# Kernel tuning notes

Measured on AMD Instinct MI355X. Metric: run time of the kernel, lower is better.

Reference implementation:

```python
import math
import jax, jax.numpy as jnp
import numpy as np

HEADS = 16
REL_WINDOW = 128


def setup_inputs() -> dict:
    key = jax.random.key(0)
    k1, k2, k3, k4, k5 = jax.random.split(key, 5)
    b, s, d = 2, 2048, 1024
    hd = d // HEADS          # 64
    R = 2 * REL_WINDOW + 1   # 257
    return {
        "x": jax.random.normal(k1, (b, s, d), dtype=jnp.float32),
        "Wqkv": jax.random.normal(k2, (3 * d, d), dtype=jnp.float32) * (1.0 / math.sqrt(d)),
        "bqkv": jax.random.normal(k3, (3 * d,), dtype=jnp.float32) * 0.02,
        "Wr": jax.random.normal(k4, (R, hd), dtype=jnp.float32) * (1.0 / math.sqrt(hd)),
        "br": jax.random.normal(k5, (R,), dtype=jnp.float32) * 0.02,
    }


def reference(x, Wqkv, bqkv, Wr, br):
    b, s, d = x.shape
    h = HEADS
    hd = d // h
    w = REL_WINDOW
    scale = math.sqrt(d / h)

    # qkv projection; torch view(b,s,h,3*hd) then chunk(3, dim=-1)
    qkv = (x @ Wqkv.T + bqkv).reshape(b, s, h, 3 * hd)
    q, k, v = jnp.split(qkv, 3, axis=-1)          # each [b,s,h,hd]
    q = q.transpose(0, 2, 1, 3)                   # [b,h,s,hd]
    k = k.transpose(0, 2, 1, 3)
    v = v.transpose(0, 2, 1, 3)

    # content scores
    content = jnp.einsum('bhik,bhjk->bhij', q, k) / scale  # [b,h,s,s]

    # relative position scores: project queries to R logits, gather per (i,j) offset
    idx = jnp.arange(s)
    offsets = jnp.clip(idx[None, :] - idx[:, None], -w, w) + w  # [s,s] in [0, 2w]
    rp = jnp.einsum('bhik,rk->bhir', q, Wr) + br               # [b,h,s,R]
    pos = jnp.take_along_axis(rp, jnp.broadcast_to(offsets, (b, h, s, s)), axis=-1)

    attn = jax.nn.softmax(content + pos, axis=-1)
    out = jnp.einsum('bhij,bhjk->bhik', attn, v)  # [b,h,s,hd]
    return out.transpose(0, 2, 1, 3).reshape(b, s, d)
```

## Files before the change

kernel.cpp:

```cpp
#include <hip/hip_runtime.h>

typedef short bfrag __attribute__((ext_vector_type(8)));
typedef float f32x4 __attribute__((ext_vector_type(4)));

#define MFMA16(a, b, c) __builtin_amdgcn_mfma_f32_16x16x32_bf16((a), (b), (c), 0, 0, 0)

#define SEQ   2048
#define DMOD  1024
#define NHEAD 16
#define HDIM  64
#define RSZ   257
#define RSTRIDE 260
#define RPADN 272
#define XN    (4096*1024)
#define WN    (3072*1024)
#define LOG2E 1.44269504f

__device__ __forceinline__ unsigned short f2bf(float f) {
  unsigned int u = __float_as_uint(f);
  u += 0x7FFFu + ((u >> 16) & 1u);
  return (unsigned short)(u >> 16);
}
__device__ __forceinline__ float bf2f(unsigned short u) {
  return __uint_as_float(((unsigned int)u) << 16);
}
__device__ __forceinline__ unsigned int pkbf(float a, float b) {
#if defined(__gfx950__)
  unsigned int r;
  asm("v_cvt_pk_bf16_f32 %0, %1, %2" : "=v"(r) : "v"(a), "v"(b));
  return r;
#else
  return (unsigned int)f2bf(a) | ((unsigned int)f2bf(b) << 16);
#endif
}
__device__ __forceinline__ float fexp2(float x) {
#if __has_builtin(__builtin_amdgcn_exp2f)
  return __builtin_amdgcn_exp2f(x);
#else
  return __expf(x * 0.69314718f);
#endif
}
__device__ __forceinline__ void gl2lds16(const void* g, void* l) {
  __builtin_amdgcn_global_load_lds(
      (__attribute__((address_space(1))) void*)(g),
      (__attribute__((address_space(3))) void*)(l), 16, 0, 0);
}

__global__ __launch_bounds__(256) void cast_all(const float* __restrict__ x,
                                                const float* __restrict__ Wqkv,
                                                const float* __restrict__ Wr,
                                                unsigned short* __restrict__ xb,
                                                unsigned short* __restrict__ wb,
                                                unsigned short* __restrict__ wrb) {
  int i = (blockIdx.x * 256 + threadIdx.x) * 4;
  if (i < XN) {
    float4 v = *(const float4*)(x + i);
    ushort4 o; o.x = f2bf(v.x); o.y = f2bf(v.y); o.z = f2bf(v.z); o.w = f2bf(v.w);
    *(ushort4*)(xb + i) = o;
  } else if (i < XN + WN) {
    int j = i - XN;
    float4 v = *(const float4*)(Wqkv + j);
    ushort4 o; o.x = f2bf(v.x); o.y = f2bf(v.y); o.z = f2bf(v.z); o.w = f2bf(v.w);
    *(ushort4*)(wb + j) = o;
  } else {
    int j = i - XN - WN;
    ushort4 o;
    unsigned short t[4];
#pragma unroll
    for (int k = 0; k < 4; ++k)
      t[k] = (j + k < RSZ * HDIM) ? f2bf(Wr[j + k]) : (unsigned short)0;
    o.x = t[0]; o.y = t[1]; o.z = t[2]; o.w = t[3];
    *(ushort4*)(wrb + j) = o;
  }
}

__global__ __launch_bounds__(256) void qkv_gemm(const unsigned short* __restrict__ xb,
                                                const unsigned short* __restrict__ wb,
                                                const float* __restrict__ bqkv,
                                                unsigned short* __restrict__ qb,
                                                unsigned short* __restrict__ kbuf,
                                                unsigned short* __restrict__ vtb) {
  __shared__ unsigned short SMEM[2 * 128 * 64];
  unsigned short* As = SMEM;
  unsigned short* Bs = SMEM + 128 * 64;
  unsigned short* Vtmp = SMEM;
  const int tid = threadIdx.x;
  const int m0 = blockIdx.y * 128, n0 = blockIdx.x * 128;
  const int wave = tid >> 6, lane = tid & 63;
  const int q4 = lane >> 4, l16 = lane & 15;
  const int wm = (wave & 1) * 64, wn = (wave >> 1) * 64;
  const int sw = l16 & 7;

  f32x4 acc[4][4];
#pragma unroll
  for (int rt = 0; rt < 4; ++rt)
#pragma unroll
    for (int ct = 0; ct < 4; ++ct) acc[rt][ct] = (f32x4){0.f, 0.f, 0.f, 0.f};

  for (int k0 = 0; k0 < DMOD; k0 += 64) {
#pragma unroll
    for (int it = 0; it < 4; ++it) {
      int ch = it * 256 + tid;
      int r = ch >> 3, cl = (ch & 7) ^ (r & 7);
      gl2lds16(xb + (size_t)(m0 + r) * DMOD + k0 + cl * 8, As + ch * 8);
      gl2lds16(wb + (size_t)(n0 + r) * DMOD + k0 + cl * 8, Bs + ch * 8);
    }
    __syncthreads();
#pragma unroll
    for (int ks = 0; ks < 2; ++ks) {
      bfrag af[4], bf[4];
#pragma unroll
      for (int rt = 0; rt < 4; ++rt)
        af[rt] = *(const bfrag*)(As + (wm + rt * 16 + l16) * 64 + ((ks * 4 + q4) ^ sw) * 8);
#pragma unroll
      for (int ct = 0; ct < 4; ++ct)
        bf[ct] = *(const bfrag*)(Bs + (wn + ct * 16 + l16) * 64 + ((ks * 4 + q4) ^ sw) * 8);
#pragma unroll
      for (int rt = 0; rt < 4; ++rt)
#pragma unroll
        for (int ct = 0; ct < 4; ++ct)
          acc[rt][ct] = MFMA16(bf[ct], af[rt], acc[rt][ct]);
    }
    __syncthreads();
  }

  const int batch = m0 >> 11;
  const int sbase = m0 & 2047;
  const int r3 = blockIdx.x % 3;
  const bool hasV = (r3 != 0);
  const int nv0 = n0 + ((r3 == 2) ? 64 : 0);

#pragma unroll
  for (int ct = 0; ct < 4; ++ct) {
    int ng = n0 + wn + ct * 16 + q4 * 4;
    int hh = ng / 192;
    int rem = ng - hh * 192;
    int t = rem >> 6, dd = rem & 63;
    float4 b4 = *(const float4*)(bqkv + ng);
    if (t < 2) {
      unsigned short* dst = (t == 0) ? qb : kbuf;
      size_t rowo = ((size_t)(batch * NHEAD + hh)) * SEQ + sbase;
#pragma unroll
      for (int rt = 0; rt < 4; ++rt) {
        int m = wm + rt * 16 + l16;
        uint2 pv;
        pv.x = pkbf(acc[rt][ct][0] + b4.x, acc[rt][ct][1] + b4.y);
        pv.y = pkbf(acc[rt][ct][2] + b4.z, acc[rt][ct][3] + b4.w);
        *(uint2*)(dst + (rowo + m) * HDIM + dd) = pv;
      }
    } else {
#pragma unroll
      for (int rt = 0; rt < 4; ++rt) {
        int m = wm + rt * 16 + l16;
        Vtmp[(dd + 0) * 136 + m] = f2bf(acc[rt][ct][0] + b4.x);
        Vtmp[(dd + 1) * 136 + m] = f2bf(acc[rt][ct][1] + b4.y);
        Vtmp[(dd + 2) * 136 + m] = f2bf(acc[rt][ct][2] + b4.z);
        Vtmp[(dd + 3) * 136 + m] = f2bf(acc[rt][ct][3] + b4.w);
      }
    }
  }

  if (hasV) {
    __syncthreads();
    const int hh = nv0 / 192;
    unsigned short* vdst = vtb + ((size_t)(batch * NHEAD + hh)) * HDIM * SEQ;
#pragma unroll
    for (int it = 0; it < 4; ++it) {
      int u = it * 256 + tid;
      int dd = u >> 4, mc = u & 15;
      bfrag val = *(const bfrag*)(Vtmp + dd * 136 + mc * 8);
      *(bfrag*)(vdst + (size_t)dd * SEQ + sbase + mc * 8) = val;
    }
  }
}

__global__ __launch_bounds__(256) void rp_gemm(const unsigned short* __restrict__ qb,
                                               const unsigned short* __restrict__ wrb,
                                               const float* __restrict__ br,
                                               unsigned short* __restrict__ rp16) {
  __shared__ unsigned short WrS[RPADN * HDIM];
  __shared__ unsigned short Qs[64 * HDIM];
  const int tid = threadIdx.x;
  const size_t row0 = (size_t)blockIdx.x * 64;

  for (int i = tid; i < RPADN * HDIM / 8; i += 256)
    *(uint4*)(&WrS[i * 8]) = *(const uint4*)(&wrb[i * 8]);
  for (int i = tid; i < 512; i += 256)
    *(uint4*)(&Qs[i * 8]) = *(const uint4*)(&qb[row0 * HDIM + i * 8]);
  __syncthreads();

  const int wave = tid >> 6, lane = tid & 63;
  const int q4 = lane >> 4, l16 = lane & 15;

  bfrag af0 = *(const bfrag*)(Qs + (wave * 16 + l16) * 64 + q4 * 8);
  bfrag af1 = *(const bfrag*)(Qs + (wave * 16 + l16) * 64 + 32 + q4 * 8);

  unsigned short* rrow = rp16 + (row0 + wave * 16 + l16) * RSTRIDE;
  const float br256 = br[256];

#pragma unroll 4
  for (int ct = 0; ct < 16; ++ct) {
    f32x4 acc = (f32x4){0.f, 0.f, 0.f, 0.f};
    bfrag w0 = *(const bfrag*)(WrS + (ct * 16 + l16) * 64 + q4 * 8);
    bfrag w1 = *(const bfrag*)(WrS + (ct * 16 + l16) * 64 + 32 + q4 * 8);
    acc = MFMA16(w0, af0, acc);
    acc = MFMA16(w1, af1, acc);
    int r = ct * 16 + q4 * 4;
    float4 b4 = *(const float4*)(br + r);
    uint2 pv;
    pv.x = pkbf((acc[0] + b4.x) * LOG2E, (acc[1] + b4.y) * LOG2E);
    pv.y = pkbf((acc[2] + b4.z) * LOG2E, (acc[3] + b4.w) * LOG2E);
    *(uint2*)(rrow + r) = pv;
  }
  {
    f32x4 acc = (f32x4){0.f, 0.f, 0.f, 0.f};
    bfrag w0 = *(const bfrag*)(WrS + (256 + l16) * 64 + q4 * 8);
    bfrag w1 = *(const bfrag*)(WrS + (256 + l16) * 64 + 32 + q4 * 8);
    acc = MFMA16(w0, af0, acc);
    acc = MFMA16(w1, af1, acc);
    if (q4 == 0)
      rrow[256] = f2bf((acc[0] + br256) * LOG2E);
  }
}

__global__ __launch_bounds__(256) void flash_attn(const unsigned short* __restrict__ qb,
                                                  const unsigned short* __restrict__ kbuf,
                                                  const unsigned short* __restrict__ vtb,
                                                  const unsigned short* __restrict__ rp16,
                                                  float* __restrict__ out) {
  __shared__ unsigned short Ks[2][64 * 64];
  __shared__ unsigned short Vs[2][64 * 64];
  __shared__ unsigned short Ps[64 * 64];

  const int tid = threadIdx.x;
  const int orig = blockIdx.x;
  const int slot = orig >> 3;
  const int bh = (orig & 7) * 4 + (slot >> 5);
  const int i0 = (slot & 31) << 6;
  const int wave = tid >> 6, lane = tid & 63;
  const int q4 = lane >> 4, l16 = lane & 15;
  const int sw = l16 & 7;
  const float SC = 0.125f * LOG2E;

  const int rloc = wave * 16 + l16;
  const int ig = i0 + rloc;
  const unsigned short* qrow = qb + ((size_t)bh * SEQ + ig) * HDIM;
  bfrag qf0 = *(const bfrag*)(qrow + q4 * 8);
  bfrag qf1 = *(const bfrag*)(qrow + 32 + q4 * 8);

  const unsigned short* rpbase = rp16 + ((size_t)bh * SEQ + ig) * RSTRIDE;
  const float rpL = bf2f(rpbase[0]);
  const float rpR = bf2f(rpbase[256]);

  float m_s = -3.0e38f, l_s = 0.f;
  f32x4 oacc[4];
#pragma unroll
  for (int ct = 0; ct < 4; ++ct) oacc[ct] = (f32x4){0.f, 0.f, 0.f, 0.f};

  const unsigned short* kbase = kbuf + (size_t)bh * SEQ * HDIM;
  const unsigned short* vbase = vtb + (size_t)bh * HDIM * SEQ;

  auto STAGE = [&](int jt, int buf) {
    const int j0s = jt * 64;
#pragma unroll
    for (int it = 0; it < 2; ++it) {
      int ch = it * 256 + tid;
      int r = ch >> 3, cl = (ch & 7) ^ (r & 7);
      gl2lds16(kbase + (size_t)(j0s + r) * HDIM + cl * 8, &Ks[buf][ch * 8]);
      gl2lds16(vbase + (size_t)r * SEQ + j0s + cl * 8, &Vs[buf][ch * 8]);
    }
  };

  STAGE(0, 0);

  for (int jt = 0; jt < 32; ++jt) {
    const int cur = jt & 1;
    const int j0 = jt * 64;

    if (jt < 31) {
      STAGE(jt + 1, cur ^ 1);
      asm volatile("s_waitcnt vmcnt(4)" ::: "memory");
    } else {
      asm volatile("s_waitcnt vmcnt(0)" ::: "memory");
    }
    __builtin_amdgcn_s_barrier();
    asm volatile("" ::: "memory");

    f32x4 sacc[4];
    __builtin_amdgcn_s_setprio(1);
#pragma unroll
    for (int ct = 0; ct < 4; ++ct) {
      sacc[ct] = (f32x4){0.f, 0.f, 0.f, 0.f};
      bfrag k0f = *(const bfrag*)(&Ks[cur][(ct * 16 + l16) * 64 + (q4 ^ sw) * 8]);
      bfrag k1f = *(const bfrag*)(&Ks[cur][(ct * 16 + l16) * 64 + ((4 + q4) ^ sw) * 8]);
      sacc[ct] = MFMA16(k0f, qf0, sacc[ct]);
      sacc[ct] = MFMA16(k1f, qf1, sacc[ct]);
    }
    __builtin_amdgcn_s_setprio(0);

    float p[4][4];
    const int dj = j0 - i0;
    if (dj >= 191) {
#pragma unroll
      for (int ct = 0; ct < 4; ++ct)
#pragma unroll
        for (int reg = 0; reg < 4; ++reg)
          p[ct][reg] = sacc[ct][reg] * SC + rpR;
    } else if (dj <= -191) {
#pragma unroll
      for (int ct = 0; ct < 4; ++ct)
#pragma unroll
        for (int reg = 0; reg < 4; ++reg)
          p[ct][reg] = sacc[ct][reg] * SC + rpL;
    } else {
#pragma unroll
      for (int ct = 0; ct < 4; ++ct) {
#pragma unroll
        for (int reg = 0; reg < 4; ++reg) {
          int j = j0 + ct * 16 + q4 * 4 + reg;
          int off = j - ig;
          off = (off < -128) ? -128 : (off > 128 ? 128 : off);
          p[ct][reg] = sacc[ct][reg] * SC + bf2f(rpbase[off + 128]);
        }
      }
    }

    float mm;
    {
      float a0 = fmaxf(fmaxf(p[0][0], p[0][1]), fmaxf(p[0][2], p[0][3]));
      float a1 = fmaxf(fmaxf(p[1][0], p[1][1]), fmaxf(p[1][2], p[1][3]));
      float a2 = fmaxf(fmaxf(p[2][0], p[2][1]), fmaxf(p[2][2], p[2][3]));
      float a3 = fmaxf(fmaxf(p[3][0], p[3][1]), fmaxf(p[3][2], p[3][3]));
      mm = fmaxf(fmaxf(a0, a1), fmaxf(a2, a3));
      mm = fmaxf(mm, __shfl_xor(mm, 16));
      mm = fmaxf(mm, __shfl_xor(mm, 32));
    }
    if (!__all(mm <= m_s + 8.0f)) {
      const float mnew = fmaxf(m_s, mm);
      const float alpha = fexp2(m_s - mnew);
      m_s = mnew;
      l_s *= alpha;
#pragma unroll
      for (int ct = 0; ct < 4; ++ct)
#pragma unroll
        for (int reg = 0; reg < 4; ++reg)
          oacc[ct][reg] *= alpha;
    }
#pragma unroll
    for (int ct = 0; ct < 4; ++ct)
#pragma unroll
      for (int reg = 0; reg < 4; ++reg)
        p[ct][reg] = fexp2(p[ct][reg] - m_s);
    {
      float s0 = (p[0][0] + p[0][1]) + (p[0][2] + p[0][3]);
      float s1 = (p[1][0] + p[1][1]) + (p[1][2] + p[1][3]);
      float s2 = (p[2][0] + p[2][1]) + (p[2][2] + p[2][3]);
      float s3 = (p[3][0] + p[3][1]) + (p[3][2] + p[3][3]);
      float rs = (s0 + s1) + (s2 + s3);
      rs += __shfl_xor(rs, 16);
      rs += __shfl_xor(rs, 32);
      l_s += rs;
    }

    unsigned int* Pw = (unsigned int*)Ps;
#pragma unroll
    for (int ct = 0; ct < 4; ++ct) {
      unsigned int pk01 = pkbf(p[ct][0], p[ct][1]);
      unsigned int pk23 = pkbf(p[ct][2], p[ct][3]);
      int chunk = ct * 2 + (q4 >> 1);
      unsigned int a = rloc * 32 + ((chunk ^ sw) << 2) + ((q4 & 1) << 1);
      Pw[a] = pk01;
      Pw[a + 1] = pk23;
    }

    bfrag pf0 = *(const bfrag*)(Ps + rloc * 64 + (q4 ^ sw) * 8);
    bfrag pf1 = *(const bfrag*)(Ps + rloc * 64 + ((4 + q4) ^ sw) * 8);
    __builtin_amdgcn_s_setprio(1);
#pragma unroll
    for (int ct = 0; ct < 4; ++ct) {
      bfrag v0f = *(const bfrag*)(&Vs[cur][(ct * 16 + l16) * 64 + (q4 ^ sw) * 8]);
      bfrag v1f = *(const bfrag*)(&Vs[cur][(ct * 16 + l16) * 64 + ((4 + q4) ^ sw) * 8]);
      oacc[ct] = MFMA16(v0f, pf0, oacc[ct]);
      oacc[ct] = MFMA16(v1f, pf1, oacc[ct]);
    }
    __builtin_amdgcn_s_setprio(0);

    __builtin_amdgcn_s_barrier();
    asm volatile("" ::: "memory");
  }

  const int bidx = bh >> 4, hh = bh & 15;
  const float inv = 1.0f / l_s;
  float* orow = out + ((size_t)bidx * SEQ + ig) * DMOD + hh * HDIM;
#pragma unroll
  for (int ct = 0; ct < 4; ++ct) {
    float4 v;
    v.x = oacc[ct][0] * inv;
    v.y = oacc[ct][1] * inv;
    v.z = oacc[ct][2] * inv;
    v.w = oacc[ct][3] * inv;
    *(float4*)(orow + ct * 16 + q4 * 4) = v;
  }
}

extern "C" void kernel_launch(void* const* d_in, const int* in_sizes, int n_in,
                              void* d_out, int out_size, void* d_ws, size_t ws_size,
                              hipStream_t stream) {
  const float* x    = (const float*)d_in[0];
  const float* Wqkv = (const float*)d_in[1];
  const float* bqkv = (const float*)d_in[2];
  const float* Wr   = (const float*)d_in[3];
  const float* br   = (const float*)d_in[4];
  float* out = (float*)d_out;

  char* ws = (char*)d_ws;
  unsigned short* xb   = (unsigned short*)(ws);
  unsigned short* wb   = (unsigned short*)(ws + 8388608);
  unsigned short* qb   = (unsigned short*)(ws + 14680064);
  unsigned short* kb   = (unsigned short*)(ws + 23068672);
  unsigned short* vtb  = (unsigned short*)(ws + 31457280);
  unsigned short* wrb  = (unsigned short*)(ws + 39845888);
  unsigned short* rp16 = (unsigned short*)(ws + 39880704);

  cast_all<<<7185, 256, 0, stream>>>(x, Wqkv, Wr, xb, wb, wrb);
  qkv_gemm<<<dim3(24, 32), 256, 0, stream>>>(xb, wb, bqkv, qb, kb, vtb);
  rp_gemm<<<1024, 256, 0, stream>>>(qb, wrb, br, rp16);
  flash_attn<<<1024, 256, 0, stream>>>(qb, kb, vtb, rp16, out);
}
```

Before: 243.3 us.

## Load K/V fragments directly from global into registers, dropping LDS staging and barriers

Removes the double-buffered LDS staging of K and V tiles and the per-iteration block barriers. Each wave now loads its MFMA K and V fragments straight from global memory into registers, and the V loads are issued after the QK MFMAs so their latency can overlap that work. The relative-position band check now uses each wave's own 16-row window instead of the block's 64 rows, so more tiles take the cheap constant-bias path. In exchange, the four waves in a block each fetch the same K/V tile, which multiplies L2/global traffic, and there is no explicit prefetch of the next tile.

```diff
diff --git a/kernel.cpp b/kernel.cpp
--- a/kernel.cpp
+++ b/kernel.cpp
@@ -228,8 +228,6 @@
                                                   const unsigned short* __restrict__ vtb,
                                                   const unsigned short* __restrict__ rp16,
                                                   float* __restrict__ out) {
-  __shared__ unsigned short Ks[2][64 * 64];
-  __shared__ unsigned short Vs[2][64 * 64];
   __shared__ unsigned short Ps[64 * 64];
 
   const int tid = threadIdx.x;
@@ -244,6 +242,7 @@
 
   const int rloc = wave * 16 + l16;
   const int ig = i0 + rloc;
+  const int iw0 = i0 + wave * 16;
   const unsigned short* qrow = qb + ((size_t)bh * SEQ + ig) * HDIM;
   bfrag qf0 = *(const bfrag*)(qrow + q4 * 8);
   bfrag qf1 = *(const bfrag*)(qrow + 32 + q4 * 8);
@@ -257,56 +256,48 @@
 #pragma unroll
   for (int ct = 0; ct < 4; ++ct) oacc[ct] = (f32x4){0.f, 0.f, 0.f, 0.f};
 
-  const unsigned short* kbase = kbuf + (size_t)bh * SEQ * HDIM;
-  const unsigned short* vbase = vtb + (size_t)bh * HDIM * SEQ;
-
-  auto STAGE = [&](int jt, int buf) {
-    const int j0s = jt * 64;
-#pragma unroll
-    for (int it = 0; it < 2; ++it) {
-      int ch = it * 256 + tid;
-      int r = ch >> 3, cl = (ch & 7) ^ (r & 7);
-      gl2lds16(kbase + (size_t)(j0s + r) * HDIM + cl * 8, &Ks[buf][ch * 8]);
-      gl2lds16(vbase + (size_t)r * SEQ + j0s + cl * 8, &Vs[buf][ch * 8]);
-    }
-  };
-
-  STAGE(0, 0);
+  const unsigned short* kfp = kbuf + (size_t)bh * SEQ * HDIM + (size_t)l16 * HDIM + q4 * 8;
+  const unsigned short* vfp = vtb + (size_t)bh * HDIM * SEQ + (size_t)l16 * SEQ + q4 * 8;
 
   for (int jt = 0; jt < 32; ++jt) {
-    const int cur = jt & 1;
     const int j0 = jt * 64;
 
-    if (jt < 31) {
-      STAGE(jt + 1, cur ^ 1);
-      asm volatile("s_waitcnt vmcnt(4)" ::: "memory");
-    } else {
-      asm volatile("s_waitcnt vmcnt(0)" ::: "memory");
-    }
-    __builtin_amdgcn_s_barrier();
-    asm volatile("" ::: "memory");
+    bfrag kf[8];
+#pragma unroll
+    for (int ct = 0; ct < 4; ++ct) {
+      const unsigned short* kr = kfp + (size_t)(j0 + ct * 16) * HDIM;
+      kf[2 * ct]     = *(const bfrag*)(kr);
+      kf[2 * ct + 1] = *(const bfrag*)(kr + 32);
+    }
 
     f32x4 sacc[4];
     __builtin_amdgcn_s_setprio(1);
 #pragma unroll
     for (int ct = 0; ct < 4; ++ct) {
-      sacc[ct] = (f32x4){0.f, 0.f, 0.f, 0.f};
-      bfrag k0f = *(const bfrag*)(&Ks[cur][(ct * 16 + l16) * 64 + (q4 ^ sw) * 8]);
-      bfrag k1f = *(const bfrag*)(&Ks[cur][(ct * 16 + l16) * 64 + ((4 + q4) ^ sw) * 8]);
-      sacc[ct] = MFMA16(k0f, qf0, sacc[ct]);
-      sacc[ct] = MFMA16(k1f, qf1, sacc[ct]);
+      f32x4 z = (f32x4){0.f, 0.f, 0.f, 0.f};
+      z = MFMA16(kf[2 * ct], qf0, z);
+      z = MFMA16(kf[2 * ct + 1], qf1, z);
+      sacc[ct] = z;
     }
     __builtin_amdgcn_s_setprio(0);
 
+    bfrag vf[8];
+#pragma unroll
+    for (int ct = 0; ct < 4; ++ct) {
+      const unsigned short* vr = vfp + (size_t)(ct * 16) * SEQ + j0;
+      vf[2 * ct]     = *(const bfrag*)(vr);
+      vf[2 * ct + 1] = *(const bfrag*)(vr + 32);
+    }
+
     float p[4][4];
-    const int dj = j0 - i0;
-    if (dj >= 191) {
+    const int djw = j0 - iw0;
+    if (djw >= 143) {
 #pragma unroll
       for (int ct = 0; ct < 4; ++ct)
 #pragma unroll
         for (int reg = 0; reg < 4; ++reg)
           p[ct][reg] = sacc[ct][reg] * SC + rpR;
-    } else if (dj <= -191) {
+    } else if (djw <= -191) {
 #pragma unroll
       for (int ct = 0; ct < 4; ++ct)
 #pragma unroll
@@ -378,15 +369,10 @@
     __builtin_amdgcn_s_setprio(1);
 #pragma unroll
     for (int ct = 0; ct < 4; ++ct) {
-      bfrag v0f = *(const bfrag*)(&Vs[cur][(ct * 16 + l16) * 64 + (q4 ^ sw) * 8]);
-      bfrag v1f = *(const bfrag*)(&Vs[cur][(ct * 16 + l16) * 64 + ((4 + q4) ^ sw) * 8]);
-      oacc[ct] = MFMA16(v0f, pf0, oacc[ct]);
-      oacc[ct] = MFMA16(v1f, pf1, oacc[ct]);
+      oacc[ct] = MFMA16(vf[2 * ct], pf0, oacc[ct]);
+      oacc[ct] = MFMA16(vf[2 * ct + 1], pf1, oacc[ct]);
     }
     __builtin_amdgcn_s_setprio(0);
-
-    __builtin_amdgcn_s_barrier();
-    asm volatile("" ::: "memory");
   }
 
   const int bidx = bh >> 4, hh = bh & 15;
```

Measured after the change: 377.3 us. 1.55x slower.
